# Optimization experiments

Measured on AMD Instinct MI355X. Metric: run time of the kernel, lower is better.

The kernel has to match this reference:

```python
import jax, jax.numpy as jnp
import numpy as np

B, D, L = 512, 512, 24

def setup_inputs() -> dict:
    key = jax.random.key(0)
    k1, k2 = jax.random.split(key)
    source = jax.random.normal(k1, (B, D), dtype=jnp.float32)
    s_labels = jax.random.randint(k2, (B, L), 0, 2, dtype=jnp.int32)
    return {"source": source, "s_labels": s_labels}

def reference(source, s_labels):
    margin = 0.0
    squared = False
    # pairwise squared euclidean distances, (B, B)
    diff = source[:, None, :] - source[None, :, :]          # (B, B, D)
    dist = jnp.clip(jnp.sum(diff * diff, axis=-1), 0.0)     # (B, B)
    if not squared:
        zmask = (dist == 0.0).astype(dist.dtype)
        dist = jnp.sqrt(dist + zmask * 1e-16) * (1.0 - zmask)
    # triplet validity mask: labels[i]==labels[j] (share a label) and labels[i]!=labels[k]
    lab = s_labels.astype(jnp.float32)
    sim = (lab @ lab.T > 0).astype(jnp.float32)              # (B, B)
    mask = sim[:, :, None] * (1.0 - sim[:, None, :])         # (B, B, B)
    # euclidean branch: d_ap - (1 - margin) * d_an
    triplet = dist[:, :, None] - (1.0 - margin) * dist[:, None, :]
    triplet = jnp.clip(mask * triplet, 0.0)                  # (B, B, B)
    num_positive = jnp.sum((triplet > 1e-16).astype(jnp.float32))
    return jnp.sum(triplet) / (num_positive + 1e-16)
```

## Files before the change

### kernel.cpp

```cpp
#include <hip/hip_runtime.h>

#define BN 512
#define DD 512
#define LL 24

typedef unsigned short u16;
typedef __attribute__((ext_vector_type(8))) short short8;
typedef __attribute__((ext_vector_type(4))) float f32x4;


__device__ __forceinline__ u16 bf16_rn(float f) {
    unsigned u = __float_as_uint(f);
    return (u16)((u + 0x7FFFu + ((u >> 16) & 1u)) >> 16);
}
__device__ __forceinline__ float bf16_f(u16 h) {
    return __uint_as_float(((unsigned)h) << 16);
}

__global__ void prep_kernel(const float* __restrict__ src, const int* __restrict__ labels,
                            float* __restrict__ norms, unsigned* __restrict__ masks,
                            u16* __restrict__ Sh, u16* __restrict__ Sl,
                            float* __restrict__ accum) {
    int i = blockIdx.x;
    int lane = threadIdx.x;
    const float4* row = (const float4*)(src + (size_t)i * DD);
    float4 v0 = row[lane];
    float4 v1 = row[lane + 64];
    float s = v0.x*v0.x + v0.y*v0.y + v0.z*v0.z + v0.w*v0.w
            + v1.x*v1.x + v1.y*v1.y + v1.z*v1.z + v1.w*v1.w;

    float f[8] = {v0.x, v0.y, v0.z, v0.w, v1.x, v1.y, v1.z, v1.w};
    u16 hi[8], lo[8];
#pragma unroll
    for (int e = 0; e < 8; e++) {
        hi[e] = bf16_rn(f[e]);
        lo[e] = bf16_rn(f[e] - bf16_f(hi[e]));
    }
    size_t o0 = (size_t)i * DD + 4 * lane;
    size_t o1 = o0 + 256;
    uint2 h0 = make_uint2((unsigned)hi[0] | ((unsigned)hi[1] << 16),
                          (unsigned)hi[2] | ((unsigned)hi[3] << 16));
    uint2 h1 = make_uint2((unsigned)hi[4] | ((unsigned)hi[5] << 16),
                          (unsigned)hi[6] | ((unsigned)hi[7] << 16));
    uint2 l0 = make_uint2((unsigned)lo[0] | ((unsigned)lo[1] << 16),
                          (unsigned)lo[2] | ((unsigned)lo[3] << 16));
    uint2 l1 = make_uint2((unsigned)lo[4] | ((unsigned)lo[5] << 16),
                          (unsigned)lo[6] | ((unsigned)lo[7] << 16));
    *(uint2*)(Sh + o0) = h0;  *(uint2*)(Sh + o1) = h1;
    *(uint2*)(Sl + o0) = l0;  *(uint2*)(Sl + o1) = l1;

#pragma unroll
    for (int off = 32; off > 0; off >>= 1) s += __shfl_down(s, off);
    int lab = (lane < LL) ? labels[i * LL + lane] : 0;
    unsigned long long b = __ballot(lab != 0);
    if (lane == 0) {
        norms[i] = s;
        masks[i] = (unsigned)(b & 0xFFFFFFull);
        if (i == 0) { accum[0] = 0.0f; ((unsigned*)accum)[1] = 0u; }
    }
}

__device__ __forceinline__ float dist_val(float d2, bool diag) {
    d2 = fmaxf(d2, 0.0f);
    float d = sqrtf(d2);
    return diag ? 0.0f : d;
}

__global__ __launch_bounds__(64) void dist_mfma_kernel(
    const u16* __restrict__ Sh, const u16* __restrict__ Sl,
    const float* __restrict__ norms, float* __restrict__ Dm)
{
    const int l    = threadIdx.x;
    const int r    = l & 15;
    const int half = l >> 4;
    const int jb = blockIdx.x * 32;
    const int ib = blockIdx.y * 32;
    const int kb = half * 8;

    const u16* pA0h = Sh + (size_t)(ib + r)      * DD + kb;
    const u16* pA1h = Sh + (size_t)(ib + 16 + r) * DD + kb;
    const u16* pB0h = Sh + (size_t)(jb + r)      * DD + kb;
    const u16* pB1h = Sh + (size_t)(jb + 16 + r) * DD + kb;
    const u16* pA0l = Sl + (size_t)(ib + r)      * DD + kb;
    const u16* pA1l = Sl + (size_t)(ib + 16 + r) * DD + kb;
    const u16* pB0l = Sl + (size_t)(jb + r)      * DD + kb;
    const u16* pB1l = Sl + (size_t)(jb + 16 + r) * DD + kb;

    f32x4 acc00 = {0.f,0.f,0.f,0.f}, acc01 = acc00, acc10 = acc00, acc11 = acc00;

    short8 a0h = *(const short8*)(pA0h), a1h = *(const short8*)(pA1h);
    short8 b0h = *(const short8*)(pB0h), b1h = *(const short8*)(pB1h);
    short8 a0l = *(const short8*)(pA0l), a1l = *(const short8*)(pA1l);
    short8 b0l = *(const short8*)(pB0l), b1l = *(const short8*)(pB1l);

    for (int k0 = 0; k0 < DD; k0 += 32) {
        short8 na0h, na1h, nb0h, nb1h, na0l, na1l, nb0l, nb1l;
        const int kn = k0 + 32;
        if (kn < DD) {
            na0h = *(const short8*)(pA0h + kn); na1h = *(const short8*)(pA1h + kn);
            nb0h = *(const short8*)(pB0h + kn); nb1h = *(const short8*)(pB1h + kn);
            na0l = *(const short8*)(pA0l + kn); na1l = *(const short8*)(pA1l + kn);
            nb0l = *(const short8*)(pB0l + kn); nb1l = *(const short8*)(pB1l + kn);
        }
        acc00 = __builtin_amdgcn_mfma_f32_16x16x32_bf16(a0h, b0h, acc00, 0, 0, 0);
        acc01 = __builtin_amdgcn_mfma_f32_16x16x32_bf16(a0h, b1h, acc01, 0, 0, 0);
        acc10 = __builtin_amdgcn_mfma_f32_16x16x32_bf16(a1h, b0h, acc10, 0, 0, 0);
        acc11 = __builtin_amdgcn_mfma_f32_16x16x32_bf16(a1h, b1h, acc11, 0, 0, 0);
        acc00 = __builtin_amdgcn_mfma_f32_16x16x32_bf16(a0h, b0l, acc00, 0, 0, 0);
        acc01 = __builtin_amdgcn_mfma_f32_16x16x32_bf16(a0h, b1l, acc01, 0, 0, 0);
        acc10 = __builtin_amdgcn_mfma_f32_16x16x32_bf16(a1h, b0l, acc10, 0, 0, 0);
        acc11 = __builtin_amdgcn_mfma_f32_16x16x32_bf16(a1h, b1l, acc11, 0, 0, 0);
        acc00 = __builtin_amdgcn_mfma_f32_16x16x32_bf16(a0l, b0h, acc00, 0, 0, 0);
        acc01 = __builtin_amdgcn_mfma_f32_16x16x32_bf16(a0l, b1h, acc01, 0, 0, 0);
        acc10 = __builtin_amdgcn_mfma_f32_16x16x32_bf16(a1l, b0h, acc10, 0, 0, 0);
        acc11 = __builtin_amdgcn_mfma_f32_16x16x32_bf16(a1l, b1h, acc11, 0, 0, 0);
        a0h = na0h; a1h = na1h; b0h = nb0h; b1h = nb1h;
        a0l = na0l; a1l = na1l; b0l = nb0l; b1l = nb1l;
    }

    const int jc0 = jb + r, jc1 = jb + 16 + r;
    const float nj0 = norms[jc0], nj1 = norms[jc1];
#pragma unroll
    for (int p = 0; p < 4; p++) {
        const int ir0 = ib + half * 4 + p;
        const int ir1 = ir0 + 16;
        const float ni0 = norms[ir0], ni1 = norms[ir1];
        Dm[(size_t)ir0 * BN + jc0] = dist_val(ni0 + nj0 - 2.f * acc00[p], ir0 == jc0);
        Dm[(size_t)ir0 * BN + jc1] = dist_val(ni0 + nj1 - 2.f * acc01[p], ir0 == jc1);
        Dm[(size_t)ir1 * BN + jc0] = dist_val(ni1 + nj0 - 2.f * acc10[p], ir1 == jc0);
        Dm[(size_t)ir1 * BN + jc1] = dist_val(ni1 + nj1 - 2.f * acc11[p], ir1 == jc1);
    }
}

__global__ void triplet_kernel(const float* __restrict__ Dm, const unsigned* __restrict__ masks,
                               float* __restrict__ accum) {
    __shared__ float pos[BN];
    __shared__ float neg[BN];
    __shared__ int pcnt, ncnt;
    __shared__ float wsum[4];
    __shared__ unsigned wcnt[4];
    const int i = blockIdx.x;
    const int t = threadIdx.x;
    const int lane = t & 63;
    const int w = t >> 6;
    if (t == 0) { pcnt = 0; ncnt = 0; }
    __syncthreads();
    const unsigned mi = masks[i];
    const float* drow = Dm + (size_t)i * BN;
    const unsigned long long ltmask = (1ull << lane) - 1ull;

    for (int j = t; j < BN; j += 256) {
        float dj = drow[j];
        bool isp = (mi & masks[j]) != 0u;
        unsigned long long bal = __ballot(isp);
        int np = __popcll(bal);
        if (np > 0) {
            int ldr = __ffsll((unsigned long long)bal) - 1;
            int base = 0;
            if (lane == ldr) base = atomicAdd(&pcnt, np);
            base = __shfl(base, ldr);
            if (isp) pos[base + __popcll(bal & ltmask)] = dj;
        }
        unsigned long long nbal = ~bal;
        int nn = 64 - np;
        if (nn > 0) {
            int ldr = __ffsll((unsigned long long)nbal) - 1;
            int base = 0;
            if (lane == ldr) base = atomicAdd(&ncnt, nn);
            base = __shfl(base, ldr);
            if (!isp) neg[base + __popcll(nbal & ltmask)] = dj;
        }
    }
    __syncthreads();

    const int P = pcnt, N = ncnt;
    float sum = 0.f;
    unsigned cnt = 0;
    for (int p = t; p < P; p += 256) {
        float a = pos[p];
        for (int n = 0; n < N; n++) {
            float v = a - neg[n];
            sum += fmaxf(v, 0.0f);
            cnt += (v > 1e-16f) ? 1u : 0u;
        }
    }
#pragma unroll
    for (int off = 32; off > 0; off >>= 1) {
        sum += __shfl_down(sum, off);
        cnt += __shfl_down(cnt, off);
    }
    if (lane == 0) { wsum[w] = sum; wcnt[w] = cnt; }
    __syncthreads();
    if (t == 0) {
        sum = wsum[0] + wsum[1] + wsum[2] + wsum[3];
        cnt = wcnt[0] + wcnt[1] + wcnt[2] + wcnt[3];
        if (sum != 0.f || cnt != 0u) {
            atomicAdd(&accum[0], sum);
            atomicAdd(&((unsigned*)accum)[1], cnt);
        }
    }
}

__global__ void finalize_kernel(const float* __restrict__ accum, float* __restrict__ out) {
    if (threadIdx.x == 0) {
        float s = accum[0];
        float c = (float)((const unsigned*)accum)[1];
        out[0] = s / (c + 1e-16f);
    }
}

extern "C" void kernel_launch(void* const* d_in, const int* in_sizes, int n_in,
                              void* d_out, int out_size, void* d_ws, size_t ws_size,
                              hipStream_t stream) {
    const float* src    = (const float*)d_in[0];
    const int*   labels = (const int*)d_in[1];
    float* ws = (float*)d_ws;
    float*    norms = ws;
    unsigned* masks = (unsigned*)(ws + BN);
    float*    Dm    = ws + 2 * BN;
    u16*      Sh    = (u16*)(ws + 2 * BN + (size_t)BN * BN);
    u16*      Sl    = Sh + (size_t)BN * DD;
    float*    accum = ws + 2 * BN + (size_t)BN * BN + BN * DD;

    hipLaunchKernelGGL(prep_kernel,      dim3(BN),     dim3(64),  0, stream,
                       src, labels, norms, masks, Sh, Sl, accum);
    hipLaunchKernelGGL(dist_mfma_kernel, dim3(16, 16), dim3(64),  0, stream,
                       Sh, Sl, norms, Dm);
    hipLaunchKernelGGL(triplet_kernel,   dim3(BN),     dim3(256), 0, stream,
                       Dm, masks, accum);
    hipLaunchKernelGGL(finalize_kernel,  dim3(1),      dim3(64),  0, stream,
                       accum, (float*)d_out);
}
```

Before: 75.10 us.

## Fuse bf16 split, norms and label masks into the MFMA distance kernel

Removes the separate prep kernel. The distance kernel now loads fp32 rows directly, splits them into hi/lo bf16 in registers, and accumulates the row norms during the k loop, combining them with shuffles. Label masks and the accumulator reset move into the blockIdx.y==0 blocks. This saves one kernel launch and the round trip of the bf16 copies through memory. In exchange, each block re-converts its rows redundantly, reads twice as many bytes per element (fp32 instead of bf16), and holds more registers.

```diff
diff --git a/kernel.cpp b/kernel.cpp
--- a/kernel.cpp
+++ b/kernel.cpp
@@ -15,49 +15,6 @@
 }
 __device__ __forceinline__ float bf16_f(u16 h) {
     return __uint_as_float(((unsigned)h) << 16);
-}
-
-__global__ void prep_kernel(const float* __restrict__ src, const int* __restrict__ labels,
-                            float* __restrict__ norms, unsigned* __restrict__ masks,
-                            u16* __restrict__ Sh, u16* __restrict__ Sl,
-                            float* __restrict__ accum) {
-    int i = blockIdx.x;
-    int lane = threadIdx.x;
-    const float4* row = (const float4*)(src + (size_t)i * DD);
-    float4 v0 = row[lane];
-    float4 v1 = row[lane + 64];
-    float s = v0.x*v0.x + v0.y*v0.y + v0.z*v0.z + v0.w*v0.w
-            + v1.x*v1.x + v1.y*v1.y + v1.z*v1.z + v1.w*v1.w;
-
-    float f[8] = {v0.x, v0.y, v0.z, v0.w, v1.x, v1.y, v1.z, v1.w};
-    u16 hi[8], lo[8];
-#pragma unroll
-    for (int e = 0; e < 8; e++) {
-        hi[e] = bf16_rn(f[e]);
-        lo[e] = bf16_rn(f[e] - bf16_f(hi[e]));
-    }
-    size_t o0 = (size_t)i * DD + 4 * lane;
-    size_t o1 = o0 + 256;
-    uint2 h0 = make_uint2((unsigned)hi[0] | ((unsigned)hi[1] << 16),
-                          (unsigned)hi[2] | ((unsigned)hi[3] << 16));
-    uint2 h1 = make_uint2((unsigned)hi[4] | ((unsigned)hi[5] << 16),
-                          (unsigned)hi[6] | ((unsigned)hi[7] << 16));
-    uint2 l0 = make_uint2((unsigned)lo[0] | ((unsigned)lo[1] << 16),
-                          (unsigned)lo[2] | ((unsigned)lo[3] << 16));
-    uint2 l1 = make_uint2((unsigned)lo[4] | ((unsigned)lo[5] << 16),
-                          (unsigned)lo[6] | ((unsigned)lo[7] << 16));
-    *(uint2*)(Sh + o0) = h0;  *(uint2*)(Sh + o1) = h1;
-    *(uint2*)(Sl + o0) = l0;  *(uint2*)(Sl + o1) = l1;
-
-#pragma unroll
-    for (int off = 32; off > 0; off >>= 1) s += __shfl_down(s, off);
-    int lab = (lane < LL) ? labels[i * LL + lane] : 0;
-    unsigned long long b = __ballot(lab != 0);
-    if (lane == 0) {
-        norms[i] = s;
-        masks[i] = (unsigned)(b & 0xFFFFFFull);
-        if (i == 0) { accum[0] = 0.0f; ((unsigned*)accum)[1] = 0u; }
-    }
 }
 
 __device__ __forceinline__ float dist_val(float d2, bool diag) {
@@ -66,9 +23,21 @@
     return diag ? 0.0f : d;
 }
 
-__global__ __launch_bounds__(64) void dist_mfma_kernel(
-    const u16* __restrict__ Sh, const u16* __restrict__ Sl,
-    const float* __restrict__ norms, float* __restrict__ Dm)
+__device__ __forceinline__ void split8(float4 x, float4 y, short8& h, short8& l, float& nrm) {
+    float f[8] = {x.x, x.y, x.z, x.w, y.x, y.y, y.z, y.w};
+#pragma unroll
+    for (int e = 0; e < 8; e++) {
+        nrm = fmaf(f[e], f[e], nrm);
+        u16 hb = bf16_rn(f[e]);
+        u16 lb = bf16_rn(f[e] - bf16_f(hb));
+        h[e] = (short)hb;
+        l[e] = (short)lb;
+    }
+}
+
+__global__ __launch_bounds__(64) void dist_fused_kernel(
+    const float* __restrict__ S, const int* __restrict__ labels,
+    unsigned* __restrict__ masks, float* __restrict__ Dm, float* __restrict__ accum)
 {
     const int l    = threadIdx.x;
     const int r    = l & 15;
@@ -77,31 +46,45 @@
     const int ib = blockIdx.y * 32;
     const int kb = half * 8;
 
-    const u16* pA0h = Sh + (size_t)(ib + r)      * DD + kb;
-    const u16* pA1h = Sh + (size_t)(ib + 16 + r) * DD + kb;
-    const u16* pB0h = Sh + (size_t)(jb + r)      * DD + kb;
-    const u16* pB1h = Sh + (size_t)(jb + 16 + r) * DD + kb;
-    const u16* pA0l = Sl + (size_t)(ib + r)      * DD + kb;
-    const u16* pA1l = Sl + (size_t)(ib + 16 + r) * DD + kb;
-    const u16* pB0l = Sl + (size_t)(jb + r)      * DD + kb;
-    const u16* pB1l = Sl + (size_t)(jb + 16 + r) * DD + kb;
+    if (blockIdx.y == 0) {
+        if (l < 32) {
+            const int row = blockIdx.x * 32 + l;
+            const int* lab = labels + row * LL;
+            unsigned m = 0;
+#pragma unroll
+            for (int q = 0; q < LL; q++) m |= (lab[q] != 0 ? 1u : 0u) << q;
+            masks[row] = m;
+        }
+        if (blockIdx.x == 0 && l == 0) { accum[0] = 0.0f; ((unsigned*)accum)[1] = 0u; }
+    }
+
+    const float* pA0 = S + (size_t)(ib + r)      * DD + kb;
+    const float* pA1 = S + (size_t)(ib + 16 + r) * DD + kb;
+    const float* pB0 = S + (size_t)(jb + r)      * DD + kb;
+    const float* pB1 = S + (size_t)(jb + 16 + r) * DD + kb;
 
     f32x4 acc00 = {0.f,0.f,0.f,0.f}, acc01 = acc00, acc10 = acc00, acc11 = acc00;
-
-    short8 a0h = *(const short8*)(pA0h), a1h = *(const short8*)(pA1h);
-    short8 b0h = *(const short8*)(pB0h), b1h = *(const short8*)(pB1h);
-    short8 a0l = *(const short8*)(pA0l), a1l = *(const short8*)(pA1l);
-    short8 b0l = *(const short8*)(pB0l), b1l = *(const short8*)(pB1l);
+    float nA0 = 0.f, nA1 = 0.f, nB0 = 0.f, nB1 = 0.f;
+
+    float4 a0x = *(const float4*)pA0, a0y = *(const float4*)(pA0 + 4);
+    float4 a1x = *(const float4*)pA1, a1y = *(const float4*)(pA1 + 4);
+    float4 b0x = *(const float4*)pB0, b0y = *(const float4*)(pB0 + 4);
+    float4 b1x = *(const float4*)pB1, b1y = *(const float4*)(pB1 + 4);
 
     for (int k0 = 0; k0 < DD; k0 += 32) {
-        short8 na0h, na1h, nb0h, nb1h, na0l, na1l, nb0l, nb1l;
+        float4 na0x, na0y, na1x, na1y, nb0x, nb0y, nb1x, nb1y;
         const int kn = k0 + 32;
         if (kn < DD) {
-            na0h = *(const short8*)(pA0h + kn); na1h = *(const short8*)(pA1h + kn);
-            nb0h = *(const short8*)(pB0h + kn); nb1h = *(const short8*)(pB1h + kn);
-            na0l = *(const short8*)(pA0l + kn); na1l = *(const short8*)(pA1l + kn);
-            nb0l = *(const short8*)(pB0l + kn); nb1l = *(const short8*)(pB1l + kn);
-        }
+            na0x = *(const float4*)(pA0 + kn); na0y = *(const float4*)(pA0 + kn + 4);
+            na1x = *(const float4*)(pA1 + kn); na1y = *(const float4*)(pA1 + kn + 4);
+            nb0x = *(const float4*)(pB0 + kn); nb0y = *(const float4*)(pB0 + kn + 4);
+            nb1x = *(const float4*)(pB1 + kn); nb1y = *(const float4*)(pB1 + kn + 4);
+        }
+        short8 a0h, a0l, a1h, a1l, b0h, b0l, b1h, b1l;
+        split8(a0x, a0y, a0h, a0l, nA0);
+        split8(a1x, a1y, a1h, a1l, nA1);
+        split8(b0x, b0y, b0h, b0l, nB0);
+        split8(b1x, b1y, b1h, b1l, nB1);
         acc00 = __builtin_amdgcn_mfma_f32_16x16x32_bf16(a0h, b0h, acc00, 0, 0, 0);
         acc01 = __builtin_amdgcn_mfma_f32_16x16x32_bf16(a0h, b1h, acc01, 0, 0, 0);
         acc10 = __builtin_amdgcn_mfma_f32_16x16x32_bf16(a1h, b0h, acc10, 0, 0, 0);
@@ -114,17 +97,23 @@
         acc01 = __builtin_amdgcn_mfma_f32_16x16x32_bf16(a0l, b1h, acc01, 0, 0, 0);
         acc10 = __builtin_amdgcn_mfma_f32_16x16x32_bf16(a1l, b0h, acc10, 0, 0, 0);
         acc11 = __builtin_amdgcn_mfma_f32_16x16x32_bf16(a1l, b1h, acc11, 0, 0, 0);
-        a0h = na0h; a1h = na1h; b0h = nb0h; b1h = nb1h;
-        a0l = na0l; a1l = na1l; b0l = nb0l; b1l = nb1l;
-    }
+        a0x = na0x; a0y = na0y; a1x = na1x; a1y = na1y;
+        b0x = nb0x; b0y = nb0y; b1x = nb1x; b1y = nb1y;
+    }
+
+    nA0 += __shfl_xor(nA0, 16); nA0 += __shfl_xor(nA0, 32);
+    nA1 += __shfl_xor(nA1, 16); nA1 += __shfl_xor(nA1, 32);
+    nB0 += __shfl_xor(nB0, 16); nB0 += __shfl_xor(nB0, 32);
+    nB1 += __shfl_xor(nB1, 16); nB1 += __shfl_xor(nB1, 32);
 
     const int jc0 = jb + r, jc1 = jb + 16 + r;
-    const float nj0 = norms[jc0], nj1 = norms[jc1];
+    const float nj0 = nB0, nj1 = nB1;
 #pragma unroll
     for (int p = 0; p < 4; p++) {
         const int ir0 = ib + half * 4 + p;
         const int ir1 = ir0 + 16;
-        const float ni0 = norms[ir0], ni1 = norms[ir1];
+        const float ni0 = __shfl(nA0, half * 4 + p);
+        const float ni1 = __shfl(nA1, half * 4 + p);
         Dm[(size_t)ir0 * BN + jc0] = dist_val(ni0 + nj0 - 2.f * acc00[p], ir0 == jc0);
         Dm[(size_t)ir0 * BN + jc1] = dist_val(ni0 + nj1 - 2.f * acc01[p], ir0 == jc1);
         Dm[(size_t)ir1 * BN + jc0] = dist_val(ni1 + nj0 - 2.f * acc10[p], ir1 == jc0);
@@ -215,19 +204,14 @@
     const float* src    = (const float*)d_in[0];
     const int*   labels = (const int*)d_in[1];
     float* ws = (float*)d_ws;
-    float*    norms = ws;
-    unsigned* masks = (unsigned*)(ws + BN);
-    float*    Dm    = ws + 2 * BN;
-    u16*      Sh    = (u16*)(ws + 2 * BN + (size_t)BN * BN);
-    u16*      Sl    = Sh + (size_t)BN * DD;
-    float*    accum = ws + 2 * BN + (size_t)BN * BN + BN * DD;
-
-    hipLaunchKernelGGL(prep_kernel,      dim3(BN),     dim3(64),  0, stream,
-                       src, labels, norms, masks, Sh, Sl, accum);
-    hipLaunchKernelGGL(dist_mfma_kernel, dim3(16, 16), dim3(64),  0, stream,
-                       Sh, Sl, norms, Dm);
-    hipLaunchKernelGGL(triplet_kernel,   dim3(BN),     dim3(256), 0, stream,
+    unsigned* masks = (unsigned*)ws;
+    float*    Dm    = ws + BN;
+    float*    accum = ws + BN + (size_t)BN * BN;
+
+    hipLaunchKernelGGL(dist_fused_kernel, dim3(16, 16), dim3(64),  0, stream,
+                       src, labels, masks, Dm, accum);
+    hipLaunchKernelGGL(triplet_kernel,    dim3(BN),     dim3(256), 0, stream,
                        Dm, masks, accum);
-    hipLaunchKernelGGL(finalize_kernel,  dim3(1),      dim3(64),  0, stream,
+    hipLaunchKernelGGL(finalize_kernel,   dim3(1),      dim3(64),  0, stream,
                        accum, (float*)d_out);
 }
```

Result: no change. 76.50 us (+1.9%).
